# Kernel tuning notes

Measured on AMD Instinct MI355X. Metric: run time of the kernel, lower is better.

The kernel has to match this reference:

```python
import jax, jax.numpy as jnp
import numpy as np
import math

TAU = 1.0  # init kwarg tau


def setup_inputs() -> dict:
    key = jax.random.key(0)
    n, m = 1024, 8192
    V = jax.random.normal(key, (n, m), dtype=jnp.float32)
    return {"V": V}


def reference(V) -> jnp.ndarray:
    n, m = V.shape
    num_rounds = math.ceil(m / n)
    # Repeat V row-blocks num_rounds times: M has shape [num_rounds*n, m]
    M = jnp.tile(V, (num_rounds, 1))

    def step(c, row):
        # Soft round-robin pick (training branch of SoftRR.__one_round)
        y = jax.nn.softmax((row - jnp.min(row) + 1.0) * c / TAU)
        c = (1.0 - y) * c
        return c, y

    c0 = jnp.ones((m,), dtype=V.dtype)
    _, R = jax.lax.scan(step, c0, M)  # R: [num_rounds*n, m]
    pi = R.reshape(num_rounds, n, m).sum(axis=0)  # [n, m]
    return pi
```

## Files before the change

kernel.cpp:

```cpp
#include <hip/hip_runtime.h>
#include <hip/hip_fp16.h>


#define N_ROWS 1024
#define M_COLS 8192
#define STEPS  8192
#define LOG2E  1.4426950408889634f

using half8  = __attribute__((ext_vector_type(8))) _Float16;
using half2v = __attribute__((ext_vector_type(2))) _Float16;
using f32x2  = __attribute__((ext_vector_type(2))) float;

__device__ __forceinline__ float fast_exp2(float x) {
#if __has_builtin(__builtin_amdgcn_exp2f)
  return __builtin_amdgcn_exp2f(x);
#else
  return exp2f(x);
#endif
}
__device__ __forceinline__ float fast_rcp(float x) {
#if __has_builtin(__builtin_amdgcn_rcpf)
  return __builtin_amdgcn_rcpf(x);
#else
  return 1.0f / x;
#endif
}
__device__ __forceinline__ half2v pack_f16(float y0, float y1) {
  return __builtin_bit_cast(half2v, __builtin_amdgcn_cvt_pkrtz(y0, y1));
}

template <int CTRL>
__device__ __forceinline__ float dpp_add(float x) {
  int yi = __builtin_amdgcn_update_dpp(0, __builtin_bit_cast(int, x),
                                       CTRL, 0xf, 0xf, true);
  return x + __builtin_bit_cast(float, yi);
}

__device__ __forceinline__ float wave_sum_to_lane63(float x) {
  x = dpp_add<0x111>(x);
  x = dpp_add<0x112>(x);
  x = dpp_add<0x114>(x);
  x = dpp_add<0x118>(x);
  x = dpp_add<0x142>(x);
  x = dpp_add<0x143>(x);
  return x;
}

#define BAR_LDS_ONLY() asm volatile("s_waitcnt lgkmcnt(0)\n\ts_barrier" ::: "memory")

__global__ void softrr_rowmin(const float* __restrict__ V, float* __restrict__ rmin) {
  const int row = blockIdx.x;
  const float* p = V + (size_t)row * M_COLS;
  float m = 1e30f;
  for (int j = threadIdx.x; j < M_COLS; j += 256) m = fminf(m, p[j]);
#pragma unroll
  for (int off = 32; off; off >>= 1) m = fminf(m, __shfl_xor(m, off, 64));
  __shared__ float sm[4];
  if ((threadIdx.x & 63) == 0) sm[threadIdx.x >> 6] = m;
  __syncthreads();
  if (threadIdx.x == 0) {
    rmin[row] = fminf(fminf(sm[0], sm[1]), fminf(sm[2], sm[3]));
  }
}

__global__ void softrr_prep_perm(const float* __restrict__ V, const float* __restrict__ rmin,
                                 __half* __restrict__ A) {
  const int gid = blockIdx.x * 256 + threadIdx.x;
  const int row = gid >> 10;
  const int pc  = gid & 1023;
  const int q   = pc >> 8;
  const int tt  = pc & 255;
  const int cc  = 4 * tt + q;
  const float mn = rmin[row];
  const float4* V4 = (const float4*)V;
  float4 va = V4[row * 2048 + 2 * cc];
  float4 vb = V4[row * 2048 + 2 * cc + 1];
  half8 o;
  o[0] = (_Float16)((va.x - mn + 1.0f) * LOG2E);
  o[1] = (_Float16)((va.y - mn + 1.0f) * LOG2E);
  o[2] = (_Float16)((va.z - mn + 1.0f) * LOG2E);
  o[3] = (_Float16)((va.w - mn + 1.0f) * LOG2E);
  o[4] = (_Float16)((vb.x - mn + 1.0f) * LOG2E);
  o[5] = (_Float16)((vb.y - mn + 1.0f) * LOG2E);
  o[6] = (_Float16)((vb.z - mn + 1.0f) * LOG2E);
  o[7] = (_Float16)((vb.w - mn + 1.0f) * LOG2E);
  ((half8*)A)[gid] = o;
}

__global__ void __launch_bounds__(256) softrr_scan4(const __half* __restrict__ Ah,
                                                    __half* __restrict__ Eh,
                                                    float* __restrict__ SinvW) {
  const int t = threadIdx.x;
  const int wave = t >> 6;
  const int lane = t & 63;
  __shared__ __align__(16) float sP[2][4];

  const half8* __restrict__ A8 = (const half8*)Ah;
  half8* __restrict__ E8 = (half8*)Eh;

  f32x2 c[16];
#pragma unroll
  for (int k = 0; k < 16; ++k) c[k] = (f32x2){1.0f, 1.0f};

  half8 X[4], Y[4];
#pragma unroll
  for (int q = 0; q < 4; ++q) X[q] = A8[q * 256 + t];
#pragma unroll
  for (int q = 0; q < 4; ++q) Y[q] = A8[1024 + q * 256 + t];

  unsigned aoffE = 2 * 1024, aoffO = 3 * 1024;
  unsigned eoffE = 0,        eoffO = 1024;

  auto half_step = [&](half8 (&B)[4], unsigned aoff, unsigned eoff, int par, int s) {
    f32x2 e[16];
#pragma unroll
    for (int q = 0; q < 4; ++q) {
#pragma unroll
      for (int j = 0; j < 4; ++j) {
        const int k = q * 4 + j;
        e[k][0] = fast_exp2((float)B[q][2 * j]     * c[k][0]);
        e[k][1] = fast_exp2((float)B[q][2 * j + 1] * c[k][1]);
      }
    }
#pragma unroll
    for (int q = 0; q < 4; ++q) B[q] = A8[aoff + q * 256 + t];

#pragma unroll
    for (int q = 0; q < 4; ++q) {
      half8 o;
#pragma unroll
      for (int j = 0; j < 4; ++j) {
        half2v h = pack_f16(e[q * 4 + j][0], e[q * 4 + j][1]);
        o[2 * j] = h[0]; o[2 * j + 1] = h[1];
      }
      E8[eoff + q * 256 + t] = o;
    }

    f32x2 u0 = (e[0] + e[1]) + (e[2] + e[3]);
    f32x2 u1 = (e[4] + e[5]) + (e[6] + e[7]);
    f32x2 u2 = (e[8] + e[9]) + (e[10] + e[11]);
    f32x2 u3 = (e[12] + e[13]) + (e[14] + e[15]);
    f32x2 tw = (u0 + u1) + (u2 + u3);
    float l = tw[0] + tw[1];

    l = wave_sum_to_lane63(l);
    if (lane == 63) sP[par][wave] = l;
    BAR_LDS_ONLY();

    float4 p4 = *(const float4*)(&sP[par][0]);
    const float S = (p4.x + p4.y) + (p4.z + p4.w);
    const float Sinv = fast_rcp(S);
    if (t == 0) SinvW[s] = Sinv;

    const f32x2 Sv = (f32x2){Sinv, Sinv};
#pragma unroll
    for (int k = 0; k < 16; ++k) {
      e[k] = c[k] * e[k];
      c[k] = c[k] - e[k] * Sv;
    }
  };

  for (int s = 0; s < STEPS; s += 2) {
    half_step(X, aoffE, eoffE, 0, s);
    aoffE = (aoffE + 2048) & (1024 * 1024 - 1);
    eoffE += 2048;
    half_step(Y, aoffO, eoffO, 1, s + 1);
    aoffO = (aoffO + 2048) & (1024 * 1024 - 1);
    eoffO += 2048;
  }
}

__global__ void softrr_sum8p(const __half* __restrict__ Eh,
                             const float* __restrict__ SinvW,
                             float* __restrict__ out) {
  const int gid = blockIdx.x * 256 + threadIdx.x;
  const int i  = gid >> 10;
  const int pc = gid & 1023;
  const int q  = pc >> 8;
  const int tt = pc & 255;
  const int cc = 4 * tt + q;
  const half8* E8 = (const half8*)Eh;

  float si[8];
#pragma unroll
  for (int r = 0; r < 8; ++r) si[r] = SinvW[r * 1024 + i];

  float acc[8];
#pragma unroll
  for (int k = 0; k < 8; ++k) acc[k] = 0.0f;
#pragma unroll
  for (int r = 0; r < 8; ++r) {
    half8 v = E8[(size_t)(r * 1024 + i) * 1024 + pc];
#pragma unroll
    for (int k = 0; k < 8; ++k) acc[k] = __builtin_fmaf((float)v[k], si[r], acc[k]);
  }
  ((float4*)out)[(size_t)i * 2048 + 2 * cc]     = make_float4(acc[0], acc[1], acc[2], acc[3]);
  ((float4*)out)[(size_t)i * 2048 + 2 * cc + 1] = make_float4(acc[4], acc[5], acc[6], acc[7]);
}

__global__ void __launch_bounds__(1024) softrr_scan_b(const float* __restrict__ V,
                                                      const float* __restrict__ rmin,
                                                      float* __restrict__ out) {
  const int t = threadIdx.x;
  const int wave = t >> 6;
  const int lane = t & 63;
  __shared__ float partials[2][16];
  __shared__ float smin[N_ROWS];
  smin[t] = rmin[t];
  __syncthreads();
  const float4* __restrict__ V4 = (const float4*)V;
  float4* O4 = (float4*)out;
  float c[8];
#pragma unroll
  for (int k = 0; k < 8; ++k) c[k] = 1.0f;
  float4 va = V4[2 * t], vb = V4[2 * t + 1];
  float4 pa, pb;
  for (int s = 0; s < STEPS; ++s) {
    const int i = s & (N_ROWS - 1);
    const int r = s >> 10;
    const int in_ = (s + 1) & (N_ROWS - 1);
    float4 van = V4[in_ * 2048 + 2 * t];
    float4 vbn = V4[in_ * 2048 + 2 * t + 1];
    const float mn = smin[i];
    const float base = (1.0f - mn) * LOG2E;
    float vv[8] = {va.x, va.y, va.z, va.w, vb.x, vb.y, vb.z, vb.w};
    float e[8];
    float l = 0.0f;
#pragma unroll
    for (int k = 0; k < 8; ++k) {
      float zb = __builtin_fmaf(vv[k], LOG2E, base);
      e[k] = fast_exp2(zb * c[k]);
      l += e[k];
    }
#pragma unroll
    for (int off = 32; off; off >>= 1) l += __shfl_xor(l, off, 64);
    if (lane == 0) partials[s & 1][wave] = l;
    __syncthreads();
    float S = 0.0f;
#pragma unroll
    for (int w = 0; w < 16; ++w) S += partials[s & 1][w];
    const float Sinv = fast_rcp(S);
    float po[8] = {pa.x, pa.y, pa.z, pa.w, pb.x, pb.y, pb.z, pb.w};
    float o[8];
#pragma unroll
    for (int k = 0; k < 8; ++k) {
      float y = e[k] * Sinv;
      c[k] = __builtin_fmaf(-y, c[k], c[k]);
      o[k] = (r > 0) ? (po[k] + y) : y;
    }
    O4[i * 2048 + 2 * t]     = make_float4(o[0], o[1], o[2], o[3]);
    O4[i * 2048 + 2 * t + 1] = make_float4(o[4], o[5], o[6], o[7]);
    va = van; vb = vbn;
    pa = O4[in_ * 2048 + 2 * t];
    pb = O4[in_ * 2048 + 2 * t + 1];
  }
}

extern "C" void kernel_launch(void* const* d_in, const int* in_sizes, int n_in,
                              void* d_out, int out_size, void* d_ws, size_t ws_size,
                              hipStream_t stream) {
  const float* V = (const float*)d_in[0];
  float* out = (float*)d_out;
  float* rmin = (float*)d_ws;

  const size_t E_BYTES = (size_t)STEPS * M_COLS * 2;
  const size_t S_BYTES = (size_t)STEPS * 4;
  const size_t need = 4096 + E_BYTES + S_BYTES;

  if (ws_size >= need) {
    __half* A    = (__half*)out;
    __half* E    = (__half*)((char*)d_ws + 4096);
    float*  Sinv = (float*)((char*)d_ws + 4096 + E_BYTES);
    softrr_rowmin<<<N_ROWS, 256, 0, stream>>>(V, rmin);
    softrr_prep_perm<<<4096, 256, 0, stream>>>(V, rmin, A);
    softrr_scan4<<<1, 256, 0, stream>>>(A, E, Sinv);
    softrr_sum8p<<<4096, 256, 0, stream>>>(E, Sinv, out);
  } else {
    softrr_rowmin<<<N_ROWS, 256, 0, stream>>>(V, rmin);
    softrr_scan_b<<<1, 1024, 0, stream>>>(V, rmin, out);
  }
}
```

Baseline: 5.012 ms.

## Replace per-step workgroup barrier with fixed-point atomic counter reduction

```diff
diff --git a/kernel.cpp b/kernel.cpp
--- a/kernel.cpp
+++ b/kernel.cpp
@@ -6,6 +6,7 @@
 #define M_COLS 8192
 #define STEPS  8192
 #define LOG2E  1.4426950408889634f
+#define FXS    1048576.0f
 
 using half8  = __attribute__((ext_vector_type(8))) _Float16;
 using half2v = __attribute__((ext_vector_type(2))) _Float16;
@@ -45,8 +46,6 @@
   x = dpp_add<0x143>(x);
   return x;
 }
-
-#define BAR_LDS_ONLY() asm volatile("s_waitcnt lgkmcnt(0)\n\ts_barrier" ::: "memory")
 
 __global__ void softrr_rowmin(const float* __restrict__ V, float* __restrict__ rmin) {
   const int row = blockIdx.x;
@@ -87,13 +86,16 @@
   ((half8*)A)[gid] = o;
 }
 
-__global__ void __launch_bounds__(256) softrr_scan4(const __half* __restrict__ Ah,
-                                                    __half* __restrict__ Eh,
-                                                    float* __restrict__ SinvW) {
+__global__ void __launch_bounds__(256) softrr_scan_t(const __half* __restrict__ Ah,
+                                                     __half* __restrict__ Eh,
+                                                     float* __restrict__ SinvW) {
   const int t = threadIdx.x;
   const int wave = t >> 6;
   const int lane = t & 63;
-  __shared__ __align__(16) float sP[2][4];
+  __shared__ unsigned long long slot[4];
+
+  if (t < 4) slot[t] = 0ULL;
+  __syncthreads();
 
   const half8* __restrict__ A8 = (const half8*)Ah;
   half8* __restrict__ E8 = (half8*)Eh;
@@ -111,7 +113,12 @@
   unsigned aoffE = 2 * 1024, aoffO = 3 * 1024;
   unsigned eoffE = 0,        eoffO = 1024;
 
-  auto half_step = [&](half8 (&B)[4], unsigned aoff, unsigned eoff, int par, int s) {
+  auto half_step = [&](half8 (&B)[4], unsigned aoff, unsigned eoff, int s) {
+    if (wave == 0 && lane == 63) {
+      __hip_atomic_store(&slot[(s + 2) & 3], 0ULL,
+                         __ATOMIC_RELAXED, __HIP_MEMORY_SCOPE_WORKGROUP);
+    }
+
     f32x2 e[16];
 #pragma unroll
     for (int q = 0; q < 4; ++q) {
@@ -142,13 +149,22 @@
     f32x2 u3 = (e[12] + e[13]) + (e[14] + e[15]);
     f32x2 tw = (u0 + u1) + (u2 + u3);
     float l = tw[0] + tw[1];
-
     l = wave_sum_to_lane63(l);
-    if (lane == 63) sP[par][wave] = l;
-    BAR_LDS_ONLY();
-
-    float4 p4 = *(const float4*)(&sP[par][0]);
-    const float S = (p4.x + p4.y) + (p4.z + p4.w);
+
+    if (lane == 63) {
+      unsigned long long pk = (1ULL << 56) | (unsigned long long)(l * FXS);
+      __hip_atomic_fetch_add(&slot[s & 3], pk,
+                             __ATOMIC_RELAXED, __HIP_MEMORY_SCOPE_WORKGROUP);
+    }
+    unsigned long long v;
+    do {
+      v = __hip_atomic_load(&slot[s & 3],
+                            __ATOMIC_RELAXED, __HIP_MEMORY_SCOPE_WORKGROUP);
+    } while ((v >> 56) != 4ULL);
+
+    const unsigned lo = (unsigned)v;
+    const unsigned hi = (unsigned)(v >> 32) & 0x00FFFFFFu;
+    const float S = (float)lo * (1.0f / FXS) + (float)hi * 4096.0f;
     const float Sinv = fast_rcp(S);
     if (t == 0) SinvW[s] = Sinv;
 
@@ -161,10 +177,10 @@
   };
 
   for (int s = 0; s < STEPS; s += 2) {
-    half_step(X, aoffE, eoffE, 0, s);
+    half_step(X, aoffE, eoffE, s);
     aoffE = (aoffE + 2048) & (1024 * 1024 - 1);
     eoffE += 2048;
-    half_step(Y, aoffO, eoffO, 1, s + 1);
+    half_step(Y, aoffO, eoffO, s + 1);
     aoffO = (aoffO + 2048) & (1024 * 1024 - 1);
     eoffO += 2048;
   }
@@ -238,7 +254,7 @@
     __syncthreads();
     float S = 0.0f;
 #pragma unroll
-    for (int w = 0; w < 16; ++w) S += partials[s & 1][w];
+    for (int ww = 0; ww < 16; ++ww) S += partials[s & 1][ww];
     const float Sinv = fast_rcp(S);
     float po[8] = {pa.x, pa.y, pa.z, pa.w, pb.x, pb.y, pb.z, pb.w};
     float o[8];
@@ -273,7 +289,7 @@
     float*  Sinv = (float*)((char*)d_ws + 4096 + E_BYTES);
     softrr_rowmin<<<N_ROWS, 256, 0, stream>>>(V, rmin);
     softrr_prep_perm<<<4096, 256, 0, stream>>>(V, rmin, A);
-    softrr_scan4<<<1, 256, 0, stream>>>(A, E, Sinv);
+    softrr_scan_t<<<1, 256, 0, stream>>>(A, E, Sinv);
     softrr_sum8p<<<4096, 256, 0, stream>>>(E, Sinv, out);
   } else {
     softrr_rowmin<<<N_ROWS, 256, 0, stream>>>(V, rmin);
```

Measured after the change: 5.856 ms. 1.17x slower.
